# Optimization experiments

Measured on AMD Instinct MI355X. Metric: run time of the kernel, lower is better.

The kernel has to match this reference:

```python
import jax, jax.numpy as jnp
import numpy as np
from jax.scipy.special import logsumexp

B, S, H, L = 64, 512, 1024, 9  # batch, seq_len, hidden_size, num_labels


def setup_inputs() -> dict:
    key = jax.random.key(0)
    ks = jax.random.split(key, 6)
    inputs = jax.random.normal(ks[0], (B, S, H), jnp.float32)
    labels = jax.random.randint(ks[1], (B, S), 0, L).astype(jnp.int64)
    mask = jnp.ones((B, S), jnp.int32)
    # fc parameters (nn.Linear(hidden_size, num_labels))
    W = jax.random.normal(ks[2], (L, H), jnp.float32) / np.sqrt(H)
    b = jnp.zeros((L,), jnp.float32)
    # CRF parameters (include_start_end_trans=True)
    trans_m = jax.random.normal(ks[3], (L, L), jnp.float32) * 0.1
    start_scores = jax.random.normal(ks[4], (L,), jnp.float32) * 0.1
    end_scores = jax.random.normal(ks[5], (L,), jnp.float32) * 0.1
    return dict(inputs=inputs, labels=labels, mask=mask, W=W, b=b,
                trans_m=trans_m, start_scores=start_scores, end_scores=end_scores)


def _crf_nll_mean(inputs, W, b, trans_m, start_scores, end_scores, labels, mask):
    # logits = fc(inputs): [B, S, L]
    logits = jnp.einsum('bsh,lh->bsl', inputs, W) + b
    feats = jnp.swapaxes(logits, 0, 1)           # [S, B, L] (fastNLP transposes)
    tags = jnp.swapaxes(labels, 0, 1)            # [S, B]
    m = jnp.swapaxes(mask, 0, 1).astype(feats.dtype)  # [S, B]
    seq_len, batch, n_tags = feats.shape

    # ---- log-partition via forward algorithm (lax.scan over time) ----
    alpha0 = feats[0] + start_scores[None, :]    # [B, L]

    def step(alpha, x):
        emit, mt = x                              # emit: [B, L], mt: [B]
        # tmp[b, i, j] = alpha[b, i] + trans_m[i, j] + emit[b, j]
        tmp = alpha[:, :, None] + trans_m[None, :, :] + emit[:, None, :]
        new = logsumexp(tmp, axis=1)              # [B, L]
        alpha = jnp.where(mt[:, None] > 0, new, alpha)
        return alpha, None

    alpha, _ = jax.lax.scan(step, alpha0, (feats[1:], m[1:]))
    norm = logsumexp(alpha + end_scores[None, :], axis=1)   # [B]

    # ---- gold path score ----
    emit = jnp.take_along_axis(feats, tags[:, :, None], axis=2)[:, :, 0] * m  # [S, B]
    trans = trans_m[tags[:-1], tags[1:]] * m[1:]                               # [S-1, B]
    score = emit.sum(0) + trans.sum(0)                                         # [B]
    last_idx = m.sum(0).astype(jnp.int32) - 1                                  # [B]
    last_tags = tags[last_idx, jnp.arange(batch)]
    score = score + start_scores[tags[0]] + end_scores[last_tags]

    # loss = crf(logits, labels, mask).mean()
    return jnp.mean(norm - score)


def reference(inputs, labels, mask, W, b, trans_m, start_scores, end_scores):
    return _crf_nll_mean(inputs, W, b, trans_m, start_scores, end_scores, labels, mask)
```

## Files before the change

kernel.cpp:

```cpp
#include <hip/hip_runtime.h>


#define BATCH 64
#define SEQ   512
#define HID   1024
#define NLAB  9
#define CHUNK 32
#define NCHUNK (SEQ / CHUNK)

__device__ __forceinline__ float exp2_fast(float x) { return __builtin_amdgcn_exp2f(x); }
__device__ __forceinline__ float log2_fast(float x) { return __builtin_amdgcn_logf(x); }

#define LOG2E 1.4426950408889634f
#define LN2   0.6931471805599453f

__global__ __launch_bounds__(256) void logits_chunk_kernel(
    const float* __restrict__ inp, const float* __restrict__ Wg,
    const float* __restrict__ bias, const float* __restrict__ trans,
    const int* __restrict__ mask, float* __restrict__ feats,
    float* __restrict__ P, float* __restrict__ out)
{
    if (blockIdx.x == 0 && threadIdx.x == 0) out[0] = 0.0f;

    __shared__ float Wl[NLAB * HID];
    __shared__ float femit[CHUNK][NLAB];
    const int tid = threadIdx.x;
    for (int s = tid; s < NLAB * HID; s += 256)
        Wl[s] = Wg[s];
    __syncthreads();

    const int lane = tid & 63;
    const int wv   = tid >> 6;
    const int p    = lane & 15;
    const int q    = lane >> 4;
    const int lrow = wv * 8 + q * 2;
    const long rowbase = (long)blockIdx.x * 32 + lrow;

    const float* r0 = inp + rowbase * HID;
    const float* r1 = r0 + HID;

    float acc0[NLAB], acc1[NLAB];
    #pragma unroll
    for (int l = 0; l < NLAB; ++l) { acc0[l] = 0.f; acc1[l] = 0.f; }

    #pragma unroll
    for (int c = 0; c < 4; ++c) {
        const int colp = c * 256 + p * 4;
        float xs0[16], xs1[16];
        #pragma unroll
        for (int qq = 0; qq < 4; ++qq) {
            ((float4*)xs0)[qq] = *(const float4*)(r0 + colp + qq * 64);
            ((float4*)xs1)[qq] = *(const float4*)(r1 + colp + qq * 64);
        }
        #pragma unroll
        for (int l = 0; l < NLAB; ++l) {
            const float* wl = &Wl[l * HID + colp];
            float a0 = acc0[l], a1 = acc1[l];
            #pragma unroll
            for (int qq = 0; qq < 4; ++qq) {
                float4 w4 = *(const float4*)(wl + qq * 64);
                float ww[4] = {w4.x, w4.y, w4.z, w4.w};
                #pragma unroll
                for (int k = 0; k < 4; ++k) {
                    a0 = fmaf(xs0[qq * 4 + k], ww[k], a0);
                    a1 = fmaf(xs1[qq * 4 + k], ww[k], a1);
                }
            }
            acc0[l] = a0; acc1[l] = a1;
        }
    }

    #pragma unroll
    for (int l = 0; l < NLAB; ++l) {
        float a0 = acc0[l], a1 = acc1[l];
        a0 += __shfl_xor(a0, 8, 64);  a1 += __shfl_xor(a1, 8, 64);
        a0 += __shfl_xor(a0, 4, 64);  a1 += __shfl_xor(a1, 4, 64);
        a0 += __shfl_xor(a0, 2, 64);  a1 += __shfl_xor(a1, 2, 64);
        a0 += __shfl_xor(a0, 1, 64);  a1 += __shfl_xor(a1, 1, 64);
        acc0[l] = a0; acc1[l] = a1;
    }
    if (p == 0) {
        float* o0 = feats + rowbase * NLAB;
        float* o1 = o0 + NLAB;
        #pragma unroll
        for (int l = 0; l < NLAB; ++l) {
            float f0 = (acc0[l] + bias[l]) * LOG2E;
            float f1 = (acc1[l] + bias[l]) * LOG2E;
            o0[l] = f0;  femit[lrow][l]     = f0;
            o1[l] = f1;  femit[lrow + 1][l] = f1;
        }
    }
    __syncthreads();

    if (wv >= 2) return;

    const int c  = blockIdx.x & (NCHUNK - 1);
    const int b  = blockIdx.x >> 4;

    int g = lane / 9;
    const int jj = lane - g * 9;
    bool act = (wv == 0) ? (g < 7) : (g < 2);
    int i = act ? (wv * 7 + g) : 0;
    const int sbase = g * 9;

    float tr[NLAB];
    #pragma unroll
    for (int k = 0; k < NLAB; ++k) tr[k] = trans[k * NLAB + jj] * LOG2E;
    const float tri = trans[i * NLAB + jj] * LOG2E;

    const int* mb = mask + b * SEQ + c * CHUNK;
    const int ts = (c == 0) ? 1 : 0;

    float a;
    {
        int m0 = mb[ts];
        float e0 = femit[ts][jj];
        float aid = (i == jj) ? 0.0f : -1e30f;
        a = (m0 > 0) ? (tri + e0) : aid;
    }

    int m_nxt = mb[ts + 1];
    for (int t = ts + 1; t < CHUNK; ++t) {
        float e = femit[t][jj];
        int  mt = m_nxt;
        if (t + 1 < CHUNK) m_nxt = mb[t + 1];
        float v[NLAB];
        #pragma unroll
        for (int k = 0; k < NLAB; ++k) v[k] = __shfl(a, sbase + k, 64) + tr[k];
        float m01 = fmaxf(v[0], v[1]), m23 = fmaxf(v[2], v[3]);
        float m45 = fmaxf(v[4], v[5]), m67 = fmaxf(v[6], v[7]);
        float mx = fmaxf(fmaxf(fmaxf(m01, m23), fmaxf(m45, m67)), v[8]);
        float s = 0.0f;
        #pragma unroll
        for (int k = 0; k < NLAB; ++k) s += exp2_fast(v[k] - mx);
        float an = mx + log2_fast(s) + e;
        a = (mt > 0) ? an : a;
    }
    if (act)
        P[(long)(b * NCHUNK + c) * 81 + i * NLAB + jj] = a;
}

__global__ __launch_bounds__(64) void final_kernel(
    const float* __restrict__ feats, const float* __restrict__ trans,
    const float* __restrict__ startv, const float* __restrict__ endv,
    const int* __restrict__ labels, const int* __restrict__ mask,
    const float* __restrict__ P, float* __restrict__ out)
{
    const int b = blockIdx.x, lane = threadIdx.x;
    const float* fb = feats + (long)b * SEQ * NLAB;
    const int* lb = labels + b * SEQ;
    const int* mb = mask + b * SEQ;

    float gsum = 0.0f; int msum = 0;
    for (int t = lane; t < SEQ; t += 64) {
        int tag = lb[t];
        int mt = mb[t];
        if (mt > 0) {
            gsum += fb[t * NLAB + tag];
            msum++;
            if (t > 0) gsum += trans[lb[t - 1] * NLAB + tag] * LOG2E;
        }
    }
    #pragma unroll
    for (int off = 32; off > 0; off >>= 1) {
        gsum += __shfl_xor(gsum, off, 64);
        msum += __shfl_xor(msum, off, 64);
    }

    const int j = lane % 9;
    float al = fb[j] + startv[j] * LOG2E;
    const float* Pb = P + (long)b * NCHUNK * 81;
    float pc[NLAB];
    #pragma unroll
    for (int i = 0; i < NLAB; ++i) pc[i] = Pb[i * NLAB + j];
    #pragma unroll
    for (int c = 0; c < NCHUNK; ++c) {
        float pn[NLAB];
        if (c < NCHUNK - 1) {
            #pragma unroll
            for (int i = 0; i < NLAB; ++i) pn[i] = Pb[(c + 1) * 81 + i * NLAB + j];
        } else {
            #pragma unroll
            for (int i = 0; i < NLAB; ++i) pn[i] = 0.0f;
        }
        float v[NLAB];
        #pragma unroll
        for (int i = 0; i < NLAB; ++i) v[i] = __shfl(al, i, 64) + pc[i];
        float m01 = fmaxf(v[0], v[1]), m23 = fmaxf(v[2], v[3]);
        float m45 = fmaxf(v[4], v[5]), m67 = fmaxf(v[6], v[7]);
        float mx = fmaxf(fmaxf(fmaxf(m01, m23), fmaxf(m45, m67)), v[8]);
        float s = 0.0f;
        #pragma unroll
        for (int i = 0; i < NLAB; ++i) s += exp2_fast(v[i] - mx);
        al = mx + log2_fast(s);
        #pragma unroll
        for (int i = 0; i < NLAB; ++i) pc[i] = pn[i];
    }
    al += endv[j] * LOG2E;

    float v[NLAB];
    #pragma unroll
    for (int i = 0; i < NLAB; ++i) v[i] = __shfl(al, i, 64);
    float m01 = fmaxf(v[0], v[1]), m23 = fmaxf(v[2], v[3]);
    float m45 = fmaxf(v[4], v[5]), m67 = fmaxf(v[6], v[7]);
    float mx = fmaxf(fmaxf(fmaxf(m01, m23), fmaxf(m45, m67)), v[8]);
    float s = 0.0f;
    #pragma unroll
    for (int i = 0; i < NLAB; ++i) s += exp2_fast(v[i] - mx);
    float norm = mx + log2_fast(s);

    if (lane == 0) {
        int li = (msum > 0) ? (msum - 1) : 0;
        float score = gsum + startv[lb[0]] * LOG2E + endv[lb[li]] * LOG2E;
        atomicAdd(out, (norm - score) * (LN2 / (float)BATCH));
    }
}

extern "C" void kernel_launch(void* const* d_in, const int* in_sizes, int n_in,
                              void* d_out, int out_size, void* d_ws, size_t ws_size,
                              hipStream_t stream)
{
    const float* inp    = (const float*)d_in[0];
    const int*   labels = (const int*)d_in[1];
    const int*   mask   = (const int*)d_in[2];
    const float* W      = (const float*)d_in[3];
    const float* bias   = (const float*)d_in[4];
    const float* trans  = (const float*)d_in[5];
    const float* startv = (const float*)d_in[6];
    const float* endv   = (const float*)d_in[7];

    float* feats = (float*)d_ws;
    float* P     = feats + BATCH * SEQ * NLAB;
    float* out   = (float*)d_out;

    hipLaunchKernelGGL(logits_chunk_kernel, dim3(BATCH * SEQ / 32), dim3(256), 0,
                       stream, inp, W, bias, trans, mask, feats, P, out);
    hipLaunchKernelGGL(final_kernel, dim3(BATCH), dim3(64), 0, stream,
                       feats, trans, startv, endv, labels, mask, P, out);
}
```

Before: 237.4 us.

## Process 64 rows per 512-thread block to amortize W staging

```diff
diff --git a/kernel.cpp b/kernel.cpp
--- a/kernel.cpp
+++ b/kernel.cpp
@@ -7,6 +7,7 @@
 #define NLAB  9
 #define CHUNK 32
 #define NCHUNK (SEQ / CHUNK)
+#define RPB   64
 
 __device__ __forceinline__ float exp2_fast(float x) { return __builtin_amdgcn_exp2f(x); }
 __device__ __forceinline__ float log2_fast(float x) { return __builtin_amdgcn_logf(x); }
@@ -14,7 +15,7 @@
 #define LOG2E 1.4426950408889634f
 #define LN2   0.6931471805599453f
 
-__global__ __launch_bounds__(256) void logits_chunk_kernel(
+__global__ __launch_bounds__(512, 4) void logits_chunk_kernel(
     const float* __restrict__ inp, const float* __restrict__ Wg,
     const float* __restrict__ bias, const float* __restrict__ trans,
     const int* __restrict__ mask, float* __restrict__ feats,
@@ -23,9 +24,9 @@
     if (blockIdx.x == 0 && threadIdx.x == 0) out[0] = 0.0f;
 
     __shared__ float Wl[NLAB * HID];
-    __shared__ float femit[CHUNK][NLAB];
+    __shared__ float femit[RPB][NLAB];
     const int tid = threadIdx.x;
-    for (int s = tid; s < NLAB * HID; s += 256)
+    for (int s = tid; s < NLAB * HID; s += 512)
         Wl[s] = Wg[s];
     __syncthreads();
 
@@ -33,74 +34,69 @@
     const int wv   = tid >> 6;
     const int p    = lane & 15;
     const int q    = lane >> 4;
-    const int lrow = wv * 8 + q * 2;
-    const long rowbase = (long)blockIdx.x * 32 + lrow;
-
-    const float* r0 = inp + rowbase * HID;
-    const float* r1 = r0 + HID;
-
-    float acc0[NLAB], acc1[NLAB];
-    #pragma unroll
-    for (int l = 0; l < NLAB; ++l) { acc0[l] = 0.f; acc1[l] = 0.f; }
-
-    #pragma unroll
-    for (int c = 0; c < 4; ++c) {
-        const int colp = c * 256 + p * 4;
-        float xs0[16], xs1[16];
-        #pragma unroll
-        for (int qq = 0; qq < 4; ++qq) {
-            ((float4*)xs0)[qq] = *(const float4*)(r0 + colp + qq * 64);
-            ((float4*)xs1)[qq] = *(const float4*)(r1 + colp + qq * 64);
-        }
+
+    float bl[NLAB];
+    #pragma unroll
+    for (int l = 0; l < NLAB; ++l) bl[l] = bias[l];
+
+    #pragma unroll 1
+    for (int pp = 0; pp < 2; ++pp) {
+        const int  lrow = wv * 8 + pp * 4 + q;
+        const long grow = (long)blockIdx.x * RPB + lrow;
+        const float* rb = inp + grow * HID + p * 4;
+        float4 xs[16];
+        #pragma unroll
+        for (int g = 0; g < 16; ++g)
+            xs[g] = *(const float4*)(rb + (g >> 2) * 256 + (g & 3) * 64);
+
+        const float* wb = Wl + p * 4;
+        float acc[NLAB];
         #pragma unroll
         for (int l = 0; l < NLAB; ++l) {
-            const float* wl = &Wl[l * HID + colp];
-            float a0 = acc0[l], a1 = acc1[l];
-            #pragma unroll
-            for (int qq = 0; qq < 4; ++qq) {
-                float4 w4 = *(const float4*)(wl + qq * 64);
-                float ww[4] = {w4.x, w4.y, w4.z, w4.w};
-                #pragma unroll
-                for (int k = 0; k < 4; ++k) {
-                    a0 = fmaf(xs0[qq * 4 + k], ww[k], a0);
-                    a1 = fmaf(xs1[qq * 4 + k], ww[k], a1);
-                }
+            float a = 0.0f;
+            #pragma unroll
+            for (int g = 0; g < 16; ++g) {
+                float4 w4 = *(const float4*)(wb + l * HID + (g >> 2) * 256 + (g & 3) * 64);
+                a = fmaf(xs[g].x, w4.x, a);
+                a = fmaf(xs[g].y, w4.y, a);
+                a = fmaf(xs[g].z, w4.z, a);
+                a = fmaf(xs[g].w, w4.w, a);
             }
-            acc0[l] = a0; acc1[l] = a1;
-        }
-    }
-
-    #pragma unroll
-    for (int l = 0; l < NLAB; ++l) {
-        float a0 = acc0[l], a1 = acc1[l];
-        a0 += __shfl_xor(a0, 8, 64);  a1 += __shfl_xor(a1, 8, 64);
-        a0 += __shfl_xor(a0, 4, 64);  a1 += __shfl_xor(a1, 4, 64);
-        a0 += __shfl_xor(a0, 2, 64);  a1 += __shfl_xor(a1, 2, 64);
-        a0 += __shfl_xor(a0, 1, 64);  a1 += __shfl_xor(a1, 1, 64);
-        acc0[l] = a0; acc1[l] = a1;
-    }
-    if (p == 0) {
-        float* o0 = feats + rowbase * NLAB;
-        float* o1 = o0 + NLAB;
+            acc[l] = a;
+        }
+
         #pragma unroll
         for (int l = 0; l < NLAB; ++l) {
-            float f0 = (acc0[l] + bias[l]) * LOG2E;
-            float f1 = (acc1[l] + bias[l]) * LOG2E;
-            o0[l] = f0;  femit[lrow][l]     = f0;
-            o1[l] = f1;  femit[lrow + 1][l] = f1;
+            float a = acc[l];
+            a += __shfl_xor(a, 8, 64);
+            a += __shfl_xor(a, 4, 64);
+            a += __shfl_xor(a, 2, 64);
+            a += __shfl_xor(a, 1, 64);
+            acc[l] = a;
+        }
+        if (p == 0) {
+            float* o = feats + grow * NLAB;
+            #pragma unroll
+            for (int l = 0; l < NLAB; ++l) {
+                float f = (acc[l] + bl[l]) * LOG2E;
+                o[l] = f;  femit[lrow][l] = f;
+            }
         }
     }
     __syncthreads();
 
-    if (wv >= 2) return;
-
-    const int c  = blockIdx.x & (NCHUNK - 1);
-    const int b  = blockIdx.x >> 4;
+    if (wv >= 4) return;
+
+    const int half = wv >> 1;
+    const int sub  = wv & 1;
+    const int b = blockIdx.x >> 3;
+    const int c = ((blockIdx.x & 7) << 1) | half;
+    const int crow0 = half * CHUNK;
 
     int g = lane / 9;
     const int jj = lane - g * 9;
-    bool act = (wv == 0) ? (g < 7) : (g < 2);
-    int i = act ? (wv * 7 + g) : 0;
+    bool act = sub ? (g < 2) : (g < 7);
+    int i = act ? (sub * 7 + g) : 0;
     const int sbase = g * 9;
 
     float tr[NLAB];
@@ -114,14 +110,14 @@
     float a;
     {
         int m0 = mb[ts];
-        float e0 = femit[ts][jj];
+        float e0 = femit[crow0 + ts][jj];
         float aid = (i == jj) ? 0.0f : -1e30f;
         a = (m0 > 0) ? (tri + e0) : aid;
     }
 
     int m_nxt = mb[ts + 1];
     for (int t = ts + 1; t < CHUNK; ++t) {
-        float e = femit[t][jj];
+        float e = femit[crow0 + t][jj];
         int  mt = m_nxt;
         if (t + 1 < CHUNK) m_nxt = mb[t + 1];
         float v[NLAB];
@@ -233,7 +229,7 @@
     float* P     = feats + BATCH * SEQ * NLAB;
     float* out   = (float*)d_out;
 
-    hipLaunchKernelGGL(logits_chunk_kernel, dim3(BATCH * SEQ / 32), dim3(256), 0,
+    hipLaunchKernelGGL(logits_chunk_kernel, dim3(BATCH * SEQ / RPB), dim3(512), 0,
                        stream, inp, W, bias, trans, mask, feats, P, out);
     hipLaunchKernelGGL(final_kernel, dim3(BATCH), dim3(64), 0, stream,
                        feats, trans, startv, endv, labels, mask, P, out);
```

New measurement: 520.9 us. +119.4%, slower.
